# Kernel tuning notes

Hardware: AMD Instinct MI355X
Metric: run time of the kernel (lower is better)

## Reference

```python
import jax, jax.numpy as jnp
import numpy as np

NUM_CLASSES = 80
NUM_ANCHORS = 3  # len(anchor_mask)
STRIDE = 8.0
# anchors[mask=0,1,2] = (12,16),(19,36),(40,28), divided by stride
ANCHOR_W = jnp.array([12.0, 19.0, 40.0], dtype=jnp.float32) / STRIDE
ANCHOR_H = jnp.array([16.0, 36.0, 28.0], dtype=jnp.float32) / STRIDE


def setup_inputs() -> dict:
    key = jax.random.key(0)
    output = jax.random.normal(key, (16, NUM_ANCHORS * (5 + NUM_CLASSES), 76, 76), dtype=jnp.float32)
    return {"output": output}


def reference(output):
    B, C_total, H, W = output.shape
    A, C = NUM_ANCHORS, NUM_CLASSES
    o = output.reshape(B, A, 5 + C, H, W)

    bxy = jax.nn.sigmoid(o[:, :, 0:2])          # [B,A,2,H,W]
    bwh = jnp.exp(o[:, :, 2:4])                 # [B,A,2,H,W]
    det_confs = jax.nn.sigmoid(o[:, :, 4])      # [B,A,H,W]
    cls_confs = jax.nn.softmax(o[:, :, 5:], axis=2)  # softmax over class dim, [B,A,C,H,W]

    grid_x = jnp.arange(W, dtype=jnp.float32)[None, None, None, :]
    grid_y = jnp.arange(H, dtype=jnp.float32)[None, None, :, None]
    aw = ANCHOR_W[None, :, None, None]
    ah = ANCHOR_H[None, :, None, None]

    bx = (bxy[:, :, 0] + grid_x) / W            # [B,A,H,W]
    by = (bxy[:, :, 1] + grid_y) / H
    bw = (bwh[:, :, 0] * aw) / W
    bh = (bwh[:, :, 1] * ah) / H

    boxes = jnp.stack([bx, by, bw, bh], axis=-1).reshape(B, A * H * W, 4)
    cls_flat = cls_confs.transpose(0, 1, 3, 4, 2).reshape(B, A * H * W, C)
    confs = cls_flat * det_confs.reshape(B, A * H * W, 1)
    return boxes, confs
```

## Files before the change

kernel.cpp:

```cpp
#include <hip/hip_runtime.h>

#define HW_   5776
#define W_    76
#define NC_   80
#define NA_   3
#define NB_   16
#define NPOS  (NB_ * NA_ * HW_)
#define ROWQ  24

__device__ __forceinline__ float sigmoidf_(float x) {
    return 1.0f / (1.0f + __expf(-x));
}

__global__ __launch_bounds__(256) void yolo_kernel(const float* __restrict__ in,
                                                   float* __restrict__ out) {
    __shared__ float4 lds[4][32 * ROWQ];

    const int tid   = threadIdx.x;
    const int lane  = tid & 63;
    const int wv    = tid >> 6;
    const int half  = lane >> 5;
    const int pos   = lane & 31;
    const int Pbase = blockIdx.x * 128 + wv * 32;
    const int P     = Pbase + pos;

    const int slab = P / HW_;
    const int p    = P - slab * HW_;
    const int a    = slab % NA_;

    const float aw3[3] = {1.5f, 2.375f, 5.0f};
    const float ah3[3] = {2.0f, 4.5f, 3.5f};
    const float invW = 1.0f / 76.0f;

    const float* src = in + (size_t)slab * (85 * (size_t)HW_) + p;

    const float b0 = src[0 * (size_t)HW_];
    const float b1 = src[1 * (size_t)HW_];
    const float b2 = src[2 * (size_t)HW_];
    const float b3 = src[3 * (size_t)HW_];
    const float b4 = src[4 * (size_t)HW_];

    const float* csrc = src + (size_t)(5 + half * 40) * HW_;
    float v[40];
#pragma unroll
    for (int c = 0; c < 40; ++c) v[c] = csrc[(size_t)c * HW_];

    const int x = p % W_;
    const int y = p / W_;
    const float bx  = (sigmoidf_(b0) + (float)x) * invW;
    const float by  = (sigmoidf_(b1) + (float)y) * invW;
    const float bw  = __expf(b2) * (aw3[a] * invW);
    const float bh  = __expf(b3) * (ah3[a] * invW);
    const float det = sigmoidf_(b4);

    float m = v[0];
#pragma unroll
    for (int c = 1; c < 40; ++c) m = fmaxf(m, v[c]);
    m = fmaxf(m, __shfl_xor(m, 32));
    float s = 0.0f;
#pragma unroll
    for (int c = 0; c < 40; ++c) { v[c] = __expf(v[c] - m); s += v[c]; }
    s += __shfl_xor(s, 32);
    const float scale = det / s;

    if (half == 0) {
        ((float4*)out)[P] = make_float4(bx, by, bw, bh);
    }

#pragma unroll
    for (int i = 0; i < 10; ++i) {
        const int k = half * 10 + i;
        const int slot = pos * ROWQ + (k ^ (pos & 7));
        lds[wv][slot] = make_float4(v[4 * i]     * scale,
                                    v[4 * i + 1] * scale,
                                    v[4 * i + 2] * scale,
                                    v[4 * i + 3] * scale);
    }

    float4* conf4 = (float4*)out + NPOS + (size_t)Pbase * 20;
#pragma unroll
    for (int i = 0; i < 10; ++i) {
        const int f     = i * 64 + lane;
        const int pos_r = f / 20;
        const int k_r   = f - pos_r * 20;
        const int slot  = pos_r * ROWQ + (k_r ^ (pos_r & 7));
        conf4[f] = lds[wv][slot];
    }
}

extern "C" void kernel_launch(void* const* d_in, const int* in_sizes, int n_in,
                              void* d_out, int out_size, void* d_ws, size_t ws_size,
                              hipStream_t stream) {
    const float* in = (const float*)d_in[0];
    float* out = (float*)d_out;
    const int nblocks = NPOS / 128;
    yolo_kernel<<<nblocks, 256, 0, stream>>>(in, out);
}
```

Measured before the change: 169.8 us.

## Stage per-slab tiles through LDS with float4 loads and nontemporal stores

Each workgroup now handles a 128-position tile within a single anchor slab. It loads all 85 channels into LDS with coalesced float4 reads, then splits each position's 80 classes across two adjacent threads that reduce via shfl_xor 1. Output stores use nontemporal hints, and the block index is swizzled across 8 groups, likely to spread work over XCDs. The last tile overlaps the previous one so HW need not be a multiple of 128. This adds a large LDS footprint and an extra barrier, which may reduce occupancy.

Measured after the change: 171.5 us. About the same (+1.0%).

```diff
diff --git a/kernel.cpp b/kernel.cpp
--- a/kernel.cpp
+++ b/kernel.cpp
@@ -2,89 +2,115 @@
 
 #define HW_   5776
 #define W_    76
-#define NC_   80
-#define NA_   3
-#define NB_   16
-#define NPOS  (NB_ * NA_ * HW_)
+#define NPOS  (16 * 3 * HW_)
+#define TPS   46
+#define NWG   (48 * TPS)
 #define ROWQ  24
+
+typedef float f32x4_ __attribute__((ext_vector_type(4)));
 
 __device__ __forceinline__ float sigmoidf_(float x) {
     return 1.0f / (1.0f + __expf(-x));
 }
 
+__device__ __forceinline__ void nt_store4(const float4& v, float4* p) {
+    __builtin_nontemporal_store(*(const f32x4_*)&v, (f32x4_*)p);
+}
+
 __global__ __launch_bounds__(256) void yolo_kernel(const float* __restrict__ in,
                                                    float* __restrict__ out) {
-    __shared__ float4 lds[4][32 * ROWQ];
+    __shared__ float4 smem[128 * ROWQ];
+    float* const sin_ = (float*)smem;
 
-    const int tid   = threadIdx.x;
-    const int lane  = tid & 63;
-    const int wv    = tid >> 6;
-    const int half  = lane >> 5;
-    const int pos   = lane & 31;
-    const int Pbase = blockIdx.x * 128 + wv * 32;
-    const int P     = Pbase + pos;
+    const int bid  = (blockIdx.x & 7) * (NWG / 8) + (blockIdx.x >> 3);
+    const int slab = bid / TPS;
+    const int tile = bid - slab * TPS;
+    const int tp   = (tile == TPS - 1) ? (HW_ - 128) : (tile << 7);
 
-    const int slab = P / HW_;
-    const int p    = P - slab * HW_;
-    const int a    = slab % NA_;
+    const int tid  = threadIdx.x;
+    const int lane = tid & 63;
+    const int wv   = tid >> 6;
+
+    const float* sbase = in + (size_t)slab * (85 * (size_t)HW_) + tp;
+
+#pragma unroll
+    for (int it = 0; it < 11; ++it) {
+        const int q = it * 256 + tid;
+        if (q < 2720) {
+            const int ch = q >> 5;
+            const int p4 = (q & 31) << 2;
+            const float4 d = *(const float4*)(sbase + (size_t)ch * HW_ + p4);
+            *(float4*)(sin_ + (ch << 7) + p4) = d;
+        }
+    }
+    __syncthreads();
+
+    const int pos  = tid >> 1;
+    const int half = tid & 1;
+    const int p    = tp + pos;
+    const int a    = slab % 3;
 
     const float aw3[3] = {1.5f, 2.375f, 5.0f};
     const float ah3[3] = {2.0f, 4.5f, 3.5f};
     const float invW = 1.0f / 76.0f;
 
-    const float* src = in + (size_t)slab * (85 * (size_t)HW_) + p;
+    const float b0 = sin_[0 * 128 + pos];
+    const float b1 = sin_[1 * 128 + pos];
+    const float b2 = sin_[2 * 128 + pos];
+    const float b3 = sin_[3 * 128 + pos];
+    const float b4 = sin_[4 * 128 + pos];
 
-    const float b0 = src[0 * (size_t)HW_];
-    const float b1 = src[1 * (size_t)HW_];
-    const float b2 = src[2 * (size_t)HW_];
-    const float b3 = src[3 * (size_t)HW_];
-    const float b4 = src[4 * (size_t)HW_];
-
-    const float* csrc = src + (size_t)(5 + half * 40) * HW_;
     float v[40];
 #pragma unroll
-    for (int c = 0; c < 40; ++c) v[c] = csrc[(size_t)c * HW_];
+    for (int c = 0; c < 40; ++c) v[c] = sin_[(5 + 40 * half + c) * 128 + pos];
 
-    const int x = p % W_;
-    const int y = p / W_;
-    const float bx  = (sigmoidf_(b0) + (float)x) * invW;
-    const float by  = (sigmoidf_(b1) + (float)y) * invW;
-    const float bw  = __expf(b2) * (aw3[a] * invW);
-    const float bh  = __expf(b3) * (ah3[a] * invW);
-    const float det = sigmoidf_(b4);
-
-    float m = v[0];
+    float m0 = v[0], m1 = v[1], m2 = v[2], m3 = v[3];
 #pragma unroll
-    for (int c = 1; c < 40; ++c) m = fmaxf(m, v[c]);
-    m = fmaxf(m, __shfl_xor(m, 32));
-    float s = 0.0f;
+    for (int c = 4; c < 40; c += 4) {
+        m0 = fmaxf(m0, v[c]);     m1 = fmaxf(m1, v[c + 1]);
+        m2 = fmaxf(m2, v[c + 2]); m3 = fmaxf(m3, v[c + 3]);
+    }
+    float m = fmaxf(fmaxf(m0, m1), fmaxf(m2, m3));
+    m = fmaxf(m, __shfl_xor(m, 1));
+    float s0 = 0.f, s1 = 0.f, s2 = 0.f, s3 = 0.f;
 #pragma unroll
-    for (int c = 0; c < 40; ++c) { v[c] = __expf(v[c] - m); s += v[c]; }
-    s += __shfl_xor(s, 32);
+    for (int c = 0; c < 40; c += 4) {
+        v[c]     = __expf(v[c]     - m); s0 += v[c];
+        v[c + 1] = __expf(v[c + 1] - m); s1 += v[c + 1];
+        v[c + 2] = __expf(v[c + 2] - m); s2 += v[c + 2];
+        v[c + 3] = __expf(v[c + 3] - m); s3 += v[c + 3];
+    }
+    float s = (s0 + s1) + (s2 + s3);
+    s += __shfl_xor(s, 1);
+    const float det   = sigmoidf_(b4);
     const float scale = det / s;
 
     if (half == 0) {
-        ((float4*)out)[P] = make_float4(bx, by, bw, bh);
+        const int x = p % W_;
+        const int y = p / W_;
+        const float bx = (sigmoidf_(b0) + (float)x) * invW;
+        const float by = (sigmoidf_(b1) + (float)y) * invW;
+        const float bw = __expf(b2) * (aw3[a] * invW);
+        const float bh = __expf(b3) * (ah3[a] * invW);
+        nt_store4(make_float4(bx, by, bw, bh), (float4*)out + slab * HW_ + p);
     }
 
+    __syncthreads();
 #pragma unroll
     for (int i = 0; i < 10; ++i) {
         const int k = half * 10 + i;
-        const int slot = pos * ROWQ + (k ^ (pos & 7));
-        lds[wv][slot] = make_float4(v[4 * i]     * scale,
-                                    v[4 * i + 1] * scale,
-                                    v[4 * i + 2] * scale,
-                                    v[4 * i + 3] * scale);
+        smem[pos * ROWQ + (k ^ (pos & 7))] =
+            make_float4(v[4 * i] * scale,     v[4 * i + 1] * scale,
+                        v[4 * i + 2] * scale, v[4 * i + 3] * scale);
     }
-
-    float4* conf4 = (float4*)out + NPOS + (size_t)Pbase * 20;
+    float4* conf4 = (float4*)out + NPOS + (size_t)(slab * HW_ + tp + wv * 32) * 20;
 #pragma unroll
     for (int i = 0; i < 10; ++i) {
-        const int f     = i * 64 + lane;
-        const int pos_r = f / 20;
-        const int k_r   = f - pos_r * 20;
-        const int slot  = pos_r * ROWQ + (k_r ^ (pos_r & 7));
-        conf4[f] = lds[wv][slot];
+        const int f   = i * 64 + lane;
+        const int pr  = f / 20;
+        const int kr  = f - pr * 20;
+        const int row = wv * 32 + pr;
+        nt_store4(smem[row * ROWQ + (kr ^ (row & 7))], conf4 + f);
     }
 }
 
@@ -93,6 +119,5 @@
                               hipStream_t stream) {
     const float* in = (const float*)d_in[0];
     float* out = (float*)d_out;
-    const int nblocks = NPOS / 128;
-    yolo_kernel<<<nblocks, 256, 0, stream>>>(in, out);
+    yolo_kernel<<<NWG, 256, 0, stream>>>(in, out);
 }
```

## Use persistent waves with double-buffered register prefetch of tiles

Applied to the files above, without the earlier changes.

Replaces the one-tile-per-wave grid with 512 persistent blocks whose waves walk tiles with a fixed stride. Each wave prefetches the next tile's 45 loads into a second register set while it processes the current one, so load latency overlaps compute. Block IDs are swizzled across groups of eight, the LDS row pitch changes to 21 in place of the XOR swizzle, and the max and sum reductions are split into four chains. Keeping two register sets roughly doubles register use, which lowers occupancy; the fixed grid may also underfill the device or balance poorly.

New measurement: 170.3 us. About the same (+0.3%).

```diff
diff --git a/kernel.cpp b/kernel.cpp
--- a/kernel.cpp
+++ b/kernel.cpp
@@ -2,89 +2,131 @@
 
 #define HW_   5776
 #define W_    76
-#define NC_   80
-#define NA_   3
-#define NB_   16
-#define NPOS  (NB_ * NA_ * HW_)
-#define ROWQ  24
+#define NPOS  (16 * 3 * HW_)
+#define NTILE (NPOS / 32)
+#define NBLK  512
+#define NWAVE (NBLK * 4)
+#define ROWQ  21
 
 __device__ __forceinline__ float sigmoidf_(float x) {
     return 1.0f / (1.0f + __expf(-x));
+}
+
+struct TileReg {
+    float b0, b1, b2, b3, b4;
+    float v[40];
+};
+
+__device__ __forceinline__ void load_tile(const float* __restrict__ in,
+                                          int P, int half, TileReg& T) {
+    const int slab = P / HW_;
+    const int p    = P - slab * HW_;
+    const float* src = in + (size_t)slab * (85 * (size_t)HW_) + p;
+    T.b0 = src[0 * (size_t)HW_];
+    T.b1 = src[1 * (size_t)HW_];
+    T.b2 = src[2 * (size_t)HW_];
+    T.b3 = src[3 * (size_t)HW_];
+    T.b4 = src[4 * (size_t)HW_];
+    const float* csrc = src + (size_t)(5 + half * 40) * HW_;
+#pragma unroll
+    for (int c = 0; c < 40; ++c) T.v[c] = csrc[(size_t)c * HW_];
+}
+
+__device__ __forceinline__ void process_tile(TileReg& T, int tile, int lane,
+                                             int half, int pos, float4* ldsw,
+                                             float* __restrict__ out) {
+    const int P    = tile * 32 + pos;
+    const int slab = P / HW_;
+    const int p    = P - slab * HW_;
+    const int a    = slab % 3;
+
+    const float aw3[3] = {1.5f, 2.375f, 5.0f};
+    const float ah3[3] = {2.0f, 4.5f, 3.5f};
+    const float invW = 1.0f / 76.0f;
+
+    float m0 = T.v[0], m1 = T.v[1], m2 = T.v[2], m3 = T.v[3];
+#pragma unroll
+    for (int c = 4; c < 40; c += 4) {
+        m0 = fmaxf(m0, T.v[c]);     m1 = fmaxf(m1, T.v[c + 1]);
+        m2 = fmaxf(m2, T.v[c + 2]); m3 = fmaxf(m3, T.v[c + 3]);
+    }
+    float m = fmaxf(fmaxf(m0, m1), fmaxf(m2, m3));
+    m = fmaxf(m, __shfl_xor(m, 32));
+    float s0 = 0.f, s1 = 0.f, s2 = 0.f, s3 = 0.f;
+#pragma unroll
+    for (int c = 0; c < 40; c += 4) {
+        T.v[c]     = __expf(T.v[c]     - m); s0 += T.v[c];
+        T.v[c + 1] = __expf(T.v[c + 1] - m); s1 += T.v[c + 1];
+        T.v[c + 2] = __expf(T.v[c + 2] - m); s2 += T.v[c + 2];
+        T.v[c + 3] = __expf(T.v[c + 3] - m); s3 += T.v[c + 3];
+    }
+    float s = (s0 + s1) + (s2 + s3);
+    s += __shfl_xor(s, 32);
+    const float det   = sigmoidf_(T.b4);
+    const float scale = det / s;
+
+    if (half == 0) {
+        const int x = p % W_;
+        const int y = p / W_;
+        const float bx = (sigmoidf_(T.b0) + (float)x) * invW;
+        const float by = (sigmoidf_(T.b1) + (float)y) * invW;
+        const float bw = __expf(T.b2) * (aw3[a] * invW);
+        const float bh = __expf(T.b3) * (ah3[a] * invW);
+        ((float4*)out)[P] = make_float4(bx, by, bw, bh);
+    }
+
+#pragma unroll
+    for (int i = 0; i < 10; ++i) {
+        const int k = half * 10 + i;
+        ldsw[pos * ROWQ + k] = make_float4(T.v[4 * i]     * scale,
+                                           T.v[4 * i + 1] * scale,
+                                           T.v[4 * i + 2] * scale,
+                                           T.v[4 * i + 3] * scale);
+    }
+    float4* conf4 = (float4*)out + NPOS + (size_t)(tile * 32) * 20;
+#pragma unroll
+    for (int i = 0; i < 10; ++i) {
+        const int f  = i * 64 + lane;
+        const int pr = f / 20;
+        const int kr = f - pr * 20;
+        conf4[f] = ldsw[pr * ROWQ + kr];
+    }
 }
 
 __global__ __launch_bounds__(256) void yolo_kernel(const float* __restrict__ in,
                                                    float* __restrict__ out) {
     __shared__ float4 lds[4][32 * ROWQ];
 
-    const int tid   = threadIdx.x;
-    const int lane  = tid & 63;
-    const int wv    = tid >> 6;
-    const int half  = lane >> 5;
-    const int pos   = lane & 31;
-    const int Pbase = blockIdx.x * 128 + wv * 32;
-    const int P     = Pbase + pos;
+    const int tid  = threadIdx.x;
+    const int lane = tid & 63;
+    const int wv   = tid >> 6;
+    const int half = lane >> 5;
+    const int pos  = lane & 31;
 
-    const int slab = P / HW_;
-    const int p    = P - slab * HW_;
-    const int a    = slab % NA_;
+    const int bid = (blockIdx.x & 7) * (NBLK / 8) + (blockIdx.x >> 3);
+    const int g   = bid * 4 + wv;
+    float4* ldsw  = lds[wv];
 
-    const float aw3[3] = {1.5f, 2.375f, 5.0f};
-    const float ah3[3] = {2.0f, 4.5f, 3.5f};
-    const float invW = 1.0f / 76.0f;
-
-    const float* src = in + (size_t)slab * (85 * (size_t)HW_) + p;
-
-    const float b0 = src[0 * (size_t)HW_];
-    const float b1 = src[1 * (size_t)HW_];
-    const float b2 = src[2 * (size_t)HW_];
-    const float b3 = src[3 * (size_t)HW_];
-    const float b4 = src[4 * (size_t)HW_];
-
-    const float* csrc = src + (size_t)(5 + half * 40) * HW_;
-    float v[40];
-#pragma unroll
-    for (int c = 0; c < 40; ++c) v[c] = csrc[(size_t)c * HW_];
-
-    const int x = p % W_;
-    const int y = p / W_;
-    const float bx  = (sigmoidf_(b0) + (float)x) * invW;
-    const float by  = (sigmoidf_(b1) + (float)y) * invW;
-    const float bw  = __expf(b2) * (aw3[a] * invW);
-    const float bh  = __expf(b3) * (ah3[a] * invW);
-    const float det = sigmoidf_(b4);
-
-    float m = v[0];
-#pragma unroll
-    for (int c = 1; c < 40; ++c) m = fmaxf(m, v[c]);
-    m = fmaxf(m, __shfl_xor(m, 32));
-    float s = 0.0f;
-#pragma unroll
-    for (int c = 0; c < 40; ++c) { v[c] = __expf(v[c] - m); s += v[c]; }
-    s += __shfl_xor(s, 32);
-    const float scale = det / s;
-
-    if (half == 0) {
-        ((float4*)out)[P] = make_float4(bx, by, bw, bh);
-    }
-
-#pragma unroll
-    for (int i = 0; i < 10; ++i) {
-        const int k = half * 10 + i;
-        const int slot = pos * ROWQ + (k ^ (pos & 7));
-        lds[wv][slot] = make_float4(v[4 * i]     * scale,
-                                    v[4 * i + 1] * scale,
-                                    v[4 * i + 2] * scale,
-                                    v[4 * i + 3] * scale);
-    }
-
-    float4* conf4 = (float4*)out + NPOS + (size_t)Pbase * 20;
-#pragma unroll
-    for (int i = 0; i < 10; ++i) {
-        const int f     = i * 64 + lane;
-        const int pos_r = f / 20;
-        const int k_r   = f - pos_r * 20;
-        const int slot  = pos_r * ROWQ + (k_r ^ (pos_r & 7));
-        conf4[f] = lds[wv][slot];
+    TileReg A, B;
+    int tA = g;
+    load_tile(in, tA * 32 + pos, half, A);
+    for (;;) {
+        const int tB = tA + NWAVE;
+        if (tB < NTILE) {
+            load_tile(in, tB * 32 + pos, half, B);
+            process_tile(A, tA, lane, half, pos, ldsw, out);
+            const int tA2 = tB + NWAVE;
+            if (tA2 < NTILE) {
+                load_tile(in, tA2 * 32 + pos, half, A);
+                process_tile(B, tB, lane, half, pos, ldsw, out);
+                tA = tA2;
+                continue;
+            }
+            process_tile(B, tB, lane, half, pos, ldsw, out);
+            break;
+        }
+        process_tile(A, tA, lane, half, pos, ldsw, out);
+        break;
     }
 }
 
@@ -93,6 +135,5 @@
                               hipStream_t stream) {
     const float* in = (const float*)d_in[0];
     float* out = (float*)d_out;
-    const int nblocks = NPOS / 128;
-    yolo_kernel<<<nblocks, 256, 0, stream>>>(in, out);
+    yolo_kernel<<<NBLK, 256, 0, stream>>>(in, out);
 }
```
